# Optimization experiments

Hardware: AMD Instinct MI355X
Metric: run time of the kernel (lower is better)

Reference implementation:

```python
import jax, jax.numpy as jnp
import numpy as np

B, L, D_IN, D_MODEL, D_STATE, D_DISCR, KER = 2, 1024, 512, 1024, 16, 64, 4


def setup_inputs() -> dict:
    ks = jax.random.split(jax.random.key(0), 9)
    s = 0.02
    return {
        "seq": jax.random.normal(ks[0], (B, L, D_IN), jnp.float32),
        "W_in": jax.random.normal(ks[1], (2 * D_MODEL, D_IN), jnp.float32) * s,
        "W_out": jax.random.normal(ks[2], (D_IN, D_MODEL), jnp.float32) * s,
        "W_B": jax.random.normal(ks[3], (D_STATE, D_MODEL), jnp.float32) * s,
        "W_C": jax.random.normal(ks[4], (D_STATE, D_MODEL), jnp.float32) * s,
        "W_D1": jax.random.normal(ks[5], (D_DISCR, D_MODEL), jnp.float32) * s,
        "W_D2": jax.random.normal(ks[6], (D_MODEL, D_DISCR), jnp.float32) * s,
        "conv_w": jax.random.normal(ks[7], (D_MODEL, 1, KER), jnp.float32) * 0.1,
        "conv_b": jax.random.normal(ks[8], (D_MODEL,), jnp.float32) * 0.01,
        "A": jnp.tile(jnp.arange(1, D_STATE + 1, dtype=jnp.float32), (D_MODEL, 1)),
        "D": jnp.ones((D_MODEL,), jnp.float32),
    }


def _causal_depthwise_conv(x, w, b):
    # x: [B, L, D] -> torch Conv1d(groups=D, padding=KER-1) truncated to first L outputs
    x = jnp.swapaxes(x, 1, 2)  # [B, D, L]
    y = jax.lax.conv_general_dilated(
        x, w, window_strides=(1,), padding=[(KER - 1, 0)],
        dimension_numbers=("NCH", "OIH", "NCH"), feature_group_count=D_MODEL)
    y = y + b[None, :, None]
    return jnp.swapaxes(y, 1, 2)  # [B, L, D]


def _ssm(x, W_B, W_C, W_D1, W_D2, A, D):
    # x: [B, L, D]
    exp_negA = jnp.exp(-A)                                  # [D, S]
    Bm = jnp.einsum("bld,sd->bls", x, W_B)                  # [B, L, S]
    Cm = jnp.einsum("bld,sd->bls", x, W_C)                  # [B, L, S]
    delta = jax.nn.softplus(D + jnp.einsum("ble,de->bld", jnp.einsum("bld,ed->ble", x, W_D1), W_D2))  # [B, L, D]
    A_bar = exp_negA[None, None] * delta[..., None]         # [B, L, D, S]
    X = Bm[:, :, None, :] * delta[..., None] * x[..., None]  # [B, L, D, S]

    def comb(c1, c2):
        a1, x1 = c1
        a2, x2 = c2
        return a1 * a2, a2 * x1 + x2

    _, h = jax.lax.associative_scan(comb, (A_bar, X), axis=1)  # h: [B, L, D, S]
    y = jnp.einsum("blds,bls->bld", h, Cm)
    return y + D * x


def reference(seq, W_in, W_out, W_B, W_C, W_D1, W_D2, conv_w, conv_b, A, D):
    ab = jnp.einsum("bli,oi->blo", seq, W_in)   # [B, L, 2*D_MODEL]
    a, b = ab[..., :D_MODEL], ab[..., D_MODEL:]
    a = jax.nn.silu(_causal_depthwise_conv(a, conv_w, conv_b))
    a = _ssm(a, W_B, W_C, W_D1, W_D2, A, D)
    out = a * jax.nn.silu(b)
    return jnp.einsum("bld,od->blo", out, W_out)  # [B, L, D_IN]
```

## Files before the change

kernel.cpp:

```cpp
#include <hip/hip_runtime.h>
#include <hip/hip_bf16.h>

typedef short short8 __attribute__((ext_vector_type(8)));
typedef float float4v __attribute__((ext_vector_type(4)));

#define B_   2
#define L_   1024
#define DIN  512
#define DM   1024
#define DS   16
#define DD   64
#define KER_ 4
#define NROW (B_*L_)

#define SD   8
#define SC   32
#define SLC  32
#define SDP  9

__device__ __forceinline__ float silu_f(float v){ return v / (1.f + expf(-v)); }

__device__ __forceinline__ short2 f2bf2(float a, float b) {
  __hip_bfloat162 h = __float22bfloat162_rn(float2{a, b});
  union { __hip_bfloat162 h; short2 s; } u; u.h = h; return u.s;
}
__device__ __forceinline__ short8 pack8(const float4& x0, const float4& x1) {
  short2 s0 = f2bf2(x0.x, x0.y), s1 = f2bf2(x0.z, x0.w);
  short2 s2 = f2bf2(x1.x, x1.y), s3 = f2bf2(x1.z, x1.w);
  return short8{ s0.x, s0.y, s1.x, s1.y, s2.x, s2.y, s3.x, s3.y };
}

__global__ __launch_bounds__(512)
void gemm1_k(const float* __restrict__ seq, const float* __restrict__ Win,
             float* __restrict__ ab) {
  __shared__ short As[128 * 40];
  __shared__ short Bs[128 * 40];
  const int tid  = threadIdx.x;
  const int lane = tid & 63;
  const int wave = tid >> 6;
  const int r16  = lane & 15;
  const int quad = lane >> 4;
  const int m0 = blockIdx.y * 128;
  const int n0 = blockIdx.x * 128;
  const int wm = wave & 1, wn = wave >> 1;
  float4v acc[4][2];
#pragma unroll
  for (int i = 0; i < 4; i++)
#pragma unroll
    for (int j = 0; j < 2; j++) acc[i][j] = (float4v){0.f, 0.f, 0.f, 0.f};
  float4 pf0[2], pf1[2];
  auto ldu = [&](int j, int k0) {
    int u = tid + j * 512;
    const float4* p;
    if (u < 512) { int row = u >> 2, q = u & 3;
      p = (const float4*)(seq + (size_t)(m0 + row) * DIN + k0 + q * 8);
    } else { int v = u - 512; int row = v >> 2, q = v & 3;
      p = (const float4*)(Win + (size_t)(n0 + row) * DIN + k0 + q * 8);
    }
    pf0[j] = p[0]; pf1[j] = p[1];
  };
  auto stu = [&](int j) {
    int u = tid + j * 512;
    short8 s = pack8(pf0[j], pf1[j]);
    if (u < 512) { int row = u >> 2, q = u & 3; *(short8*)&As[row * 40 + q * 8] = s; }
    else { int v = u - 512; int row = v >> 2, q = v & 3; *(short8*)&Bs[row * 40 + q * 8] = s; }
  };
  ldu(0, 0); ldu(1, 0);
  for (int k0 = 0; k0 < DIN; k0 += 32) {
    stu(0); stu(1);
    __syncthreads();
    if (k0 + 32 < DIN) { ldu(0, k0 + 32); ldu(1, k0 + 32); }
    short8 afr[4], bfr[2];
#pragma unroll
    for (int mi = 0; mi < 4; mi++)
      afr[mi] = *(const short8*)&As[(wm * 64 + mi * 16 + r16) * 40 + quad * 8];
#pragma unroll
    for (int ni = 0; ni < 2; ni++)
      bfr[ni] = *(const short8*)&Bs[(wn * 32 + ni * 16 + r16) * 40 + quad * 8];
#pragma unroll
    for (int mi = 0; mi < 4; mi++)
#pragma unroll
      for (int ni = 0; ni < 2; ni++)
        acc[mi][ni] = __builtin_amdgcn_mfma_f32_16x16x32_bf16(afr[mi], bfr[ni], acc[mi][ni], 0, 0, 0);
    __syncthreads();
  }
#pragma unroll
  for (int mi = 0; mi < 4; mi++)
#pragma unroll
    for (int ni = 0; ni < 2; ni++)
#pragma unroll
      for (int r = 0; r < 4; r++)
        ab[(size_t)(m0 + wm * 64 + mi * 16 + quad * 4 + r) * (2 * DM)
           + n0 + wn * 32 + ni * 16 + r16] = acc[mi][ni][r];
}

__global__ __launch_bounds__(256)
void conv_silu_k(const float* __restrict__ ab, const float* __restrict__ cw,
                 const float* __restrict__ cb, float* __restrict__ x) {
  int idx = blockIdx.x * 256 + threadIdx.x;
  int d  = idx & (DM - 1);
  int n  = idx >> 10;
  int l  = n & (L_ - 1);
  int bb = n >> 10;
  float acc = cb[d];
#pragma unroll
  for (int k = 0; k < KER_; k++) {
    int ll = l - (KER_ - 1) + k;
    if (ll >= 0) acc += ab[(size_t)(bb * L_ + ll) * (2 * DM) + d] * cw[d * KER_ + k];
  }
  x[idx] = silu_f(acc);
}

__global__ __launch_bounds__(256)
void proj_k(const float* __restrict__ x, const float* __restrict__ WB,
            const float* __restrict__ WC, const float* __restrict__ WD1,
            float* __restrict__ pall) {
  __shared__ short As[64 * 40];
  __shared__ short Bs[96 * 40];
  const int tid  = threadIdx.x;
  const int lane = tid & 63;
  const int wave = tid >> 6;
  const int r16  = lane & 15;
  const int quad = lane >> 4;
  const int m0   = blockIdx.y * 64;
  const int kbeg = blockIdx.z * 128;
  float4v acc[6];
#pragma unroll
  for (int i = 0; i < 6; i++) acc[i] = (float4v){0.f, 0.f, 0.f, 0.f};
  float4 pf0[3], pf1[3];
  auto ldu = [&](int j, int k0) {
    int u = tid + j * 256;
    if (u >= 640) return;
    const float4* p;
    if (u < 256) { int row = u >> 2, q = u & 3;
      p = (const float4*)(x + (size_t)(m0 + row) * DM + k0 + q * 8);
    } else { int v = u - 256; int row = v >> 2, q = v & 3;
      const float* bp = (row < 16) ? (WB + (size_t)row * DM)
                      : (row < 32) ? (WC + (size_t)(row - 16) * DM)
                                   : (WD1 + (size_t)(row - 32) * DM);
      p = (const float4*)(bp + k0 + q * 8);
    }
    pf0[j] = p[0]; pf1[j] = p[1];
  };
  auto stu = [&](int j) {
    int u = tid + j * 256;
    if (u >= 640) return;
    short8 s = pack8(pf0[j], pf1[j]);
    if (u < 256) { int row = u >> 2, q = u & 3; *(short8*)&As[row * 40 + q * 8] = s; }
    else { int v = u - 256; int row = v >> 2, q = v & 3; *(short8*)&Bs[row * 40 + q * 8] = s; }
  };
  ldu(0, kbeg); ldu(1, kbeg); ldu(2, kbeg);
  for (int k0 = kbeg; k0 < kbeg + 128; k0 += 32) {
    stu(0); stu(1); stu(2);
    __syncthreads();
    if (k0 + 32 < kbeg + 128) { ldu(0, k0 + 32); ldu(1, k0 + 32); ldu(2, k0 + 32); }
    short8 afr = *(const short8*)&As[(wave * 16 + r16) * 40 + quad * 8];
#pragma unroll
    for (int ni = 0; ni < 6; ni++) {
      short8 bfr = *(const short8*)&Bs[(ni * 16 + r16) * 40 + quad * 8];
      acc[ni] = __builtin_amdgcn_mfma_f32_16x16x32_bf16(afr, bfr, acc[ni], 0, 0, 0);
    }
    __syncthreads();
  }
#pragma unroll
  for (int ni = 0; ni < 6; ni++) {
    int gn = ni * 16 + r16;
#pragma unroll
    for (int r = 0; r < 4; r++) {
      int gm = m0 + wave * 16 + quad * 4 + r;
      atomicAdd(&pall[(size_t)gm * 96 + gn], acc[ni][r]);
    }
  }
}

__global__ __launch_bounds__(256)
void delta_k(const float* __restrict__ t1, const float* __restrict__ WD2,
             const float* __restrict__ Dv, float* __restrict__ dlt) {
  __shared__ short As[64 * 40];
  __shared__ short Bs[64 * 40];
  const int tid  = threadIdx.x;
  const int lane = tid & 63;
  const int wave = tid >> 6;
  const int r16  = lane & 15;
  const int quad = lane >> 4;
  const int m0 = blockIdx.y * 64;
  const int n0 = blockIdx.x * 64;
  const int wm = wave & 1, wn = wave >> 1;
  float4v acc[2][2];
#pragma unroll
  for (int i = 0; i < 2; i++)
#pragma unroll
    for (int j = 0; j < 2; j++) acc[i][j] = (float4v){0.f, 0.f, 0.f, 0.f};
  float4 pf0[2], pf1[2];
  auto ldu = [&](int j, int k0) {
    int u = tid + j * 256;
    const float4* p;
    if (u < 256) { int row = u >> 2, q = u & 3;
      p = (const float4*)(t1 + (size_t)(m0 + row) * 96 + k0 + q * 8);
    } else { int v = u - 256; int row = v >> 2, q = v & 3;
      p = (const float4*)(WD2 + (size_t)(n0 + row) * DD + k0 + q * 8);
    }
    pf0[j] = p[0]; pf1[j] = p[1];
  };
  auto stu = [&](int j) {
    int u = tid + j * 256;
    short8 s = pack8(pf0[j], pf1[j]);
    if (u < 256) { int row = u >> 2, q = u & 3; *(short8*)&As[row * 40 + q * 8] = s; }
    else { int v = u - 256; int row = v >> 2, q = v & 3; *(short8*)&Bs[row * 40 + q * 8] = s; }
  };
  ldu(0, 0); ldu(1, 0);
  for (int k0 = 0; k0 < DD; k0 += 32) {
    stu(0); stu(1);
    __syncthreads();
    if (k0 + 32 < DD) { ldu(0, k0 + 32); ldu(1, k0 + 32); }
    short8 afr[2], bfr[2];
#pragma unroll
    for (int mi = 0; mi < 2; mi++)
      afr[mi] = *(const short8*)&As[(wm * 32 + mi * 16 + r16) * 40 + quad * 8];
#pragma unroll
    for (int ni = 0; ni < 2; ni++)
      bfr[ni] = *(const short8*)&Bs[(wn * 32 + ni * 16 + r16) * 40 + quad * 8];
#pragma unroll
    for (int mi = 0; mi < 2; mi++)
#pragma unroll
      for (int ni = 0; ni < 2; ni++)
        acc[mi][ni] = __builtin_amdgcn_mfma_f32_16x16x32_bf16(afr[mi], bfr[ni], acc[mi][ni], 0, 0, 0);
    __syncthreads();
  }
#pragma unroll
  for (int mi = 0; mi < 2; mi++)
#pragma unroll
    for (int ni = 0; ni < 2; ni++) {
      int gn = n0 + wn * 32 + ni * 16 + r16;
      float dvn = Dv[gn];
#pragma unroll
      for (int r = 0; r < 4; r++) {
        int gm = m0 + wm * 32 + mi * 16 + quad * 4 + r;
        float v = acc[mi][ni][r] + dvn;
        v = fmaxf(v, 0.f) + log1pf(expf(-fabsf(v)));
        dlt[(size_t)gm * DM + gn] = v;
      }
    }
}

__global__ __launch_bounds__(256)
void scan_fused_k(const float* __restrict__ x, const float* __restrict__ dlt,
                  const float* __restrict__ pall, const float* __restrict__ A,
                  const float* __restrict__ Dv, const float* __restrict__ ab,
                  float* __restrict__ sout) {
  __shared__ float Pl[SC][DS][SDP];
  __shared__ float Hl[SC][DS][SDP];
  const int blk = blockIdx.x;
  const int b   = blk >> 7;
  const int d0  = (blk & 127) * SD;
  const int dd  = threadIdx.x & (SD - 1);
  const int c   = threadIdx.x >> 3;
  const int d   = d0 + dd;

  float e[DS];
#pragma unroll
  for (int s = 0; s < DS; s++) e[s] = expf(-A[d * DS + s]);
  const int nbase = b * L_ + c * SLC;

  float h[DS], p[DS];
#pragma unroll
  for (int s = 0; s < DS; s++) { h[s] = 0.f; p[s] = 1.f; }
  for (int i = 0; i < SLC; i++) {
    int n = nbase + i;
    float dl = dlt[(size_t)n * DM + d];
    float xv = x[(size_t)n * DM + d];
    float dx = dl * xv;
    const float4* bm4 = (const float4*)(pall + (size_t)n * 96);
    float4 b0 = bm4[0], b1 = bm4[1], b2 = bm4[2], b3 = bm4[3];
    float bmv[DS] = { b0.x,b0.y,b0.z,b0.w, b1.x,b1.y,b1.z,b1.w,
                      b2.x,b2.y,b2.z,b2.w, b3.x,b3.y,b3.z,b3.w };
#pragma unroll
    for (int s = 0; s < DS; s++) {
      float a_ = e[s] * dl;
      h[s] = a_ * h[s] + bmv[s] * dx;
      p[s] *= a_;
    }
  }
#pragma unroll
  for (int s = 0; s < DS; s++) { Pl[c][s][dd] = p[s]; Hl[c][s][dd] = h[s]; }
  __syncthreads();

  if (threadIdx.x < DS * SD) {
    int s2  = threadIdx.x >> 3;
    int dd2 = threadIdx.x & (SD - 1);
    float H = 0.f;
    for (int c2 = 0; c2 < SC; c2++) {
      float pp = Pl[c2][s2][dd2];
      float hh = Hl[c2][s2][dd2];
      Pl[c2][s2][dd2] = H;
      H = pp * H + hh;
    }
  }
  __syncthreads();

#pragma unroll
  for (int s = 0; s < DS; s++) h[s] = Pl[c][s][dd];
  float Dd = Dv[d];
  for (int i = 0; i < SLC; i++) {
    int n = nbase + i;
    float dl = dlt[(size_t)n * DM + d];
    float xv = x[(size_t)n * DM + d];
    float dx = dl * xv;
    const float4* bm4 = (const float4*)(pall + (size_t)n * 96);
    float4 b0 = bm4[0], b1 = bm4[1], b2 = bm4[2], b3 = bm4[3];
    float4 c0 = bm4[4], c1 = bm4[5], c2v = bm4[6], c3 = bm4[7];
    float bmv[DS] = { b0.x,b0.y,b0.z,b0.w, b1.x,b1.y,b1.z,b1.w,
                      b2.x,b2.y,b2.z,b2.w, b3.x,b3.y,b3.z,b3.w };
    float cmv[DS] = { c0.x,c0.y,c0.z,c0.w, c1.x,c1.y,c1.z,c1.w,
                      c2v.x,c2v.y,c2v.z,c2v.w, c3.x,c3.y,c3.z,c3.w };
    float y = 0.f;
#pragma unroll
    for (int s = 0; s < DS; s++) {
      h[s] = e[s] * dl * h[s] + bmv[s] * dx;
      y += h[s] * cmv[s];
    }
    y += Dd * xv;
    float g = ab[(size_t)n * (2 * DM) + DM + d];
    sout[(size_t)n * DM + d] = y * silu_f(g);
  }
}

__global__ __launch_bounds__(512)
void gemm2_k(const float* __restrict__ sout, const float* __restrict__ Wout,
             float* __restrict__ out) {
  __shared__ short As[64 * 40];
  __shared__ short Bs[64 * 40];
  const int tid  = threadIdx.x;
  const int lane = tid & 63;
  const int wave = tid >> 6;
  const int r16  = lane & 15;
  const int quad = lane >> 4;
  const int m0 = blockIdx.y * 64;
  const int n0 = blockIdx.x * 64;
  const int wm = wave & 1, wn = wave >> 1;
  float4v acc[2];
  acc[0] = (float4v){0.f, 0.f, 0.f, 0.f};
  acc[1] = (float4v){0.f, 0.f, 0.f, 0.f};
  float4 pf0, pf1;
  auto ldu = [&](int k0) {
    const float4* p;
    if (tid < 256) { int row = tid >> 2, q = tid & 3;
      p = (const float4*)(sout + (size_t)(m0 + row) * DM + k0 + q * 8);
    } else { int v = tid - 256; int row = v >> 2, q = v & 3;
      p = (const float4*)(Wout + (size_t)(n0 + row) * DM + k0 + q * 8);
    }
    pf0 = p[0]; pf1 = p[1];
  };
  auto stu = [&]() {
    short8 s = pack8(pf0, pf1);
    if (tid < 256) { int row = tid >> 2, q = tid & 3; *(short8*)&As[row * 40 + q * 8] = s; }
    else { int v = tid - 256; int row = v >> 2, q = v & 3; *(short8*)&Bs[row * 40 + q * 8] = s; }
  };
  ldu(0);
  for (int k0 = 0; k0 < DM; k0 += 32) {
    stu();
    __syncthreads();
    if (k0 + 32 < DM) ldu(k0 + 32);
    short8 afr[2], bfr;
    afr[0] = *(const short8*)&As[(wm * 32 + r16) * 40 + quad * 8];
    afr[1] = *(const short8*)&As[(wm * 32 + 16 + r16) * 40 + quad * 8];
    bfr    = *(const short8*)&Bs[(wn * 16 + r16) * 40 + quad * 8];
    acc[0] = __builtin_amdgcn_mfma_f32_16x16x32_bf16(afr[0], bfr, acc[0], 0, 0, 0);
    acc[1] = __builtin_amdgcn_mfma_f32_16x16x32_bf16(afr[1], bfr, acc[1], 0, 0, 0);
    __syncthreads();
  }
#pragma unroll
  for (int mi = 0; mi < 2; mi++)
#pragma unroll
    for (int r = 0; r < 4; r++)
      out[(size_t)(m0 + wm * 32 + mi * 16 + quad * 4 + r) * DIN + n0 + wn * 16 + r16] = acc[mi][r];
}

extern "C" void kernel_launch(void* const* d_in, const int* in_sizes, int n_in,
                              void* d_out, int out_size, void* d_ws, size_t ws_size,
                              hipStream_t stream) {
  const float* seq  = (const float*)d_in[0];
  const float* Win  = (const float*)d_in[1];
  const float* Wout = (const float*)d_in[2];
  const float* WB   = (const float*)d_in[3];
  const float* WC   = (const float*)d_in[4];
  const float* WD1  = (const float*)d_in[5];
  const float* WD2  = (const float*)d_in[6];
  const float* cw   = (const float*)d_in[7];
  const float* cb   = (const float*)d_in[8];
  const float* A    = (const float*)d_in[9];
  const float* Dv   = (const float*)d_in[10];
  float* out = (float*)d_out;

  float* ws   = (float*)d_ws;
  float* ab   = ws;
  float* x    = ab   + 4194304;
  float* dlt  = x    + 2097152;
  float* pall = dlt  + 2097152;
  float* sout = pall + 196608;
  float* t1   = pall + 32;

  hipMemsetAsync(pall, 0, (size_t)NROW * 96 * 4, stream);
  gemm1_k<<<dim3(16, 16), 512, 0, stream>>>(seq, Win, ab);
  conv_silu_k<<<NROW * DM / 256, 256, 0, stream>>>(ab, cw, cb, x);
  proj_k<<<dim3(1, 32, 8), 256, 0, stream>>>(x, WB, WC, WD1, pall);
  delta_k<<<dim3(16, 32), 256, 0, stream>>>(t1, WD2, Dv, dlt);
  scan_fused_k<<<B_ * (DM / SD), 256, 0, stream>>>(x, dlt, pall, A, Dv, ab, sout);
  gemm2_k<<<dim3(8, 32), 512, 0, stream>>>(sout, Wout, out);
}
```

Baseline: 179.1 us.

## Fuse causal conv+SiLU into projection and scan, store ab in bf16

Drops the standalone conv_silu kernel and its fp32 x buffer. The depthwise causal conv plus SiLU is now recomputed inside proj_k, when staging the A tile, and inside both scan passes, using a rolling three-tap register window. The gemm1 output ab is written as bf16 to halve its traffic, gemm1 moves to 64x64 tiles with 256 threads, and the scan uses 4 channels by 64 chunks per block so there are more blocks. The cost is recomputing the conv in three places and extra bf16 rounding of the gate and conv inputs.

New measurement: 179.9 us. Within noise of the previous version (+0.5%).

```diff
diff --git a/kernel.cpp b/kernel.cpp
--- a/kernel.cpp
+++ b/kernel.cpp
@@ -13,10 +13,10 @@
 #define KER_ 4
 #define NROW (B_*L_)
 
-#define SD   8
-#define SC   32
-#define SLC  32
-#define SDP  9
+#define SD   4
+#define SC   64
+#define SLC  16
+#define SDP  5
 
 __device__ __forceinline__ float silu_f(float v){ return v / (1.f + expf(-v)); }
 
@@ -29,91 +29,81 @@
   short2 s2 = f2bf2(x1.x, x1.y), s3 = f2bf2(x1.z, x1.w);
   return short8{ s0.x, s0.y, s1.x, s1.y, s2.x, s2.y, s3.x, s3.y };
 }
-
-__global__ __launch_bounds__(512)
+__device__ __forceinline__ float bf2f(short s) {
+  union { unsigned u; float f; } v; v.u = ((unsigned)(unsigned short)s) << 16; return v.f;
+}
+
+__global__ __launch_bounds__(256)
 void gemm1_k(const float* __restrict__ seq, const float* __restrict__ Win,
-             float* __restrict__ ab) {
-  __shared__ short As[128 * 40];
-  __shared__ short Bs[128 * 40];
+             __hip_bfloat16* __restrict__ ab) {
+  __shared__ short As[64 * 40];
+  __shared__ short Bs[64 * 40];
   const int tid  = threadIdx.x;
   const int lane = tid & 63;
   const int wave = tid >> 6;
   const int r16  = lane & 15;
   const int quad = lane >> 4;
-  const int m0 = blockIdx.y * 128;
-  const int n0 = blockIdx.x * 128;
+  const int m0 = blockIdx.y * 64;
+  const int n0 = blockIdx.x * 64;
   const int wm = wave & 1, wn = wave >> 1;
-  float4v acc[4][2];
-#pragma unroll
-  for (int i = 0; i < 4; i++)
+  float4v acc[2][2];
+#pragma unroll
+  for (int i = 0; i < 2; i++)
 #pragma unroll
     for (int j = 0; j < 2; j++) acc[i][j] = (float4v){0.f, 0.f, 0.f, 0.f};
   float4 pf0[2], pf1[2];
   auto ldu = [&](int j, int k0) {
-    int u = tid + j * 512;
+    int u = tid + j * 256;
     const float4* p;
-    if (u < 512) { int row = u >> 2, q = u & 3;
+    if (u < 256) { int row = u >> 2, q = u & 3;
       p = (const float4*)(seq + (size_t)(m0 + row) * DIN + k0 + q * 8);
-    } else { int v = u - 512; int row = v >> 2, q = v & 3;
+    } else { int v = u - 256; int row = v >> 2, q = v & 3;
       p = (const float4*)(Win + (size_t)(n0 + row) * DIN + k0 + q * 8);
     }
     pf0[j] = p[0]; pf1[j] = p[1];
   };
   auto stu = [&](int j) {
-    int u = tid + j * 512;
+    int u = tid + j * 256;
     short8 s = pack8(pf0[j], pf1[j]);
-    if (u < 512) { int row = u >> 2, q = u & 3; *(short8*)&As[row * 40 + q * 8] = s; }
-    else { int v = u - 512; int row = v >> 2, q = v & 3; *(short8*)&Bs[row * 40 + q * 8] = s; }
+    if (u < 256) { int row = u >> 2, q = u & 3; *(short8*)&As[row * 40 + q * 8] = s; }
+    else { int v = u - 256; int row = v >> 2, q = v & 3; *(short8*)&Bs[row * 40 + q * 8] = s; }
   };
   ldu(0, 0); ldu(1, 0);
   for (int k0 = 0; k0 < DIN; k0 += 32) {
     stu(0); stu(1);
     __syncthreads();
     if (k0 + 32 < DIN) { ldu(0, k0 + 32); ldu(1, k0 + 32); }
-    short8 afr[4], bfr[2];
-#pragma unroll
-    for (int mi = 0; mi < 4; mi++)
-      afr[mi] = *(const short8*)&As[(wm * 64 + mi * 16 + r16) * 40 + quad * 8];
+    short8 afr[2], bfr[2];
+#pragma unroll
+    for (int mi = 0; mi < 2; mi++)
+      afr[mi] = *(const short8*)&As[(wm * 32 + mi * 16 + r16) * 40 + quad * 8];
 #pragma unroll
     for (int ni = 0; ni < 2; ni++)
       bfr[ni] = *(const short8*)&Bs[(wn * 32 + ni * 16 + r16) * 40 + quad * 8];
 #pragma unroll
-    for (int mi = 0; mi < 4; mi++)
+    for (int mi = 0; mi < 2; mi++)
 #pragma unroll
       for (int ni = 0; ni < 2; ni++)
         acc[mi][ni] = __builtin_amdgcn_mfma_f32_16x16x32_bf16(afr[mi], bfr[ni], acc[mi][ni], 0, 0, 0);
     __syncthreads();
   }
 #pragma unroll
-  for (int mi = 0; mi < 4; mi++)
-#pragma unroll
-    for (int ni = 0; ni < 2; ni++)
-#pragma unroll
-      for (int r = 0; r < 4; r++)
-        ab[(size_t)(m0 + wm * 64 + mi * 16 + quad * 4 + r) * (2 * DM)
-           + n0 + wn * 32 + ni * 16 + r16] = acc[mi][ni][r];
+  for (int mi = 0; mi < 2; mi++)
+#pragma unroll
+    for (int ni = 0; ni < 2; ni++) {
+      int gn = n0 + wn * 32 + ni * 16 + r16;
+#pragma unroll
+      for (int r = 0; r < 4; r++) {
+        int gm = m0 + wm * 32 + mi * 16 + quad * 4 + r;
+        ab[(size_t)gm * (2 * DM) + gn] = __float2bfloat16(acc[mi][ni][r]);
+      }
+    }
 }
 
 __global__ __launch_bounds__(256)
-void conv_silu_k(const float* __restrict__ ab, const float* __restrict__ cw,
-                 const float* __restrict__ cb, float* __restrict__ x) {
-  int idx = blockIdx.x * 256 + threadIdx.x;
-  int d  = idx & (DM - 1);
-  int n  = idx >> 10;
-  int l  = n & (L_ - 1);
-  int bb = n >> 10;
-  float acc = cb[d];
-#pragma unroll
-  for (int k = 0; k < KER_; k++) {
-    int ll = l - (KER_ - 1) + k;
-    if (ll >= 0) acc += ab[(size_t)(bb * L_ + ll) * (2 * DM) + d] * cw[d * KER_ + k];
-  }
-  x[idx] = silu_f(acc);
-}
-
-__global__ __launch_bounds__(256)
-void proj_k(const float* __restrict__ x, const float* __restrict__ WB,
+void proj_k(const __hip_bfloat16* __restrict__ ab, const float* __restrict__ WB,
             const float* __restrict__ WC, const float* __restrict__ WD1,
+            const float* __restrict__ cw, const float* __restrict__ cb,
             float* __restrict__ pall) {
   __shared__ short As[64 * 40];
   __shared__ short Bs[96 * 40];
@@ -127,33 +117,61 @@
   float4v acc[6];
 #pragma unroll
   for (int i = 0; i < 6; i++) acc[i] = (float4v){0.f, 0.f, 0.f, 0.f};
-  float4 pf0[3], pf1[3];
-  auto ldu = [&](int j, int k0) {
+
+  short8 ta[KER_];
+  float4 pf0[2], pf1[2];
+
+  const int arow = tid >> 2, aq = tid & 3;
+  const int an = m0 + arow, al = an & (L_ - 1), abq = an >> 10;
+
+  auto ldu_a = [&](int k0) {
+#pragma unroll
+    for (int t = 0; t < KER_; t++) {
+      int ll = al - (KER_ - 1) + t;
+      if (ll >= 0)
+        ta[t] = *(const short8*)(ab + (size_t)(abq * L_ + ll) * (2 * DM) + k0 + aq * 8);
+      else
+        ta[t] = short8{0,0,0,0,0,0,0,0};
+    }
+  };
+  auto stu_a = [&](int k0) {
+    float r8[8];
+#pragma unroll
+    for (int e = 0; e < 8; e++) {
+      int d = k0 + aq * 8 + e;
+      float4 w = *(const float4*)(cw + d * 4);
+      float a = cb[d];
+      a += bf2f(ta[0][e]) * w.x;
+      a += bf2f(ta[1][e]) * w.y;
+      a += bf2f(ta[2][e]) * w.z;
+      a += bf2f(ta[3][e]) * w.w;
+      r8[e] = silu_f(a);
+    }
+    *(short8*)&As[arow * 40 + aq * 8] =
+        pack8(float4{r8[0], r8[1], r8[2], r8[3]}, float4{r8[4], r8[5], r8[6], r8[7]});
+  };
+  auto ldu_b = [&](int j, int k0) {
     int u = tid + j * 256;
     if (u >= 640) return;
-    const float4* p;
-    if (u < 256) { int row = u >> 2, q = u & 3;
-      p = (const float4*)(x + (size_t)(m0 + row) * DM + k0 + q * 8);
-    } else { int v = u - 256; int row = v >> 2, q = v & 3;
-      const float* bp = (row < 16) ? (WB + (size_t)row * DM)
-                      : (row < 32) ? (WC + (size_t)(row - 16) * DM)
-                                   : (WD1 + (size_t)(row - 32) * DM);
-      p = (const float4*)(bp + k0 + q * 8);
-    }
-    pf0[j] = p[0]; pf1[j] = p[1];
-  };
-  auto stu = [&](int j) {
+    int v = u - 256, row = v >> 2, q = v & 3;
+    const float* bp = (row < 16) ? (WB + (size_t)row * DM)
+                    : (row < 32) ? (WC + (size_t)(row - 16) * DM)
+                                 : (WD1 + (size_t)(row - 32) * DM);
+    const float4* p = (const float4*)(bp + k0 + q * 8);
+    pf0[j - 1] = p[0]; pf1[j - 1] = p[1];
+  };
+  auto stu_b = [&](int j) {
     int u = tid + j * 256;
     if (u >= 640) return;
-    short8 s = pack8(pf0[j], pf1[j]);
-    if (u < 256) { int row = u >> 2, q = u & 3; *(short8*)&As[row * 40 + q * 8] = s; }
-    else { int v = u - 256; int row = v >> 2, q = v & 3; *(short8*)&Bs[row * 40 + q * 8] = s; }
-  };
-  ldu(0, kbeg); ldu(1, kbeg); ldu(2, kbeg);
+    int v = u - 256, row = v >> 2, q = v & 3;
+    *(short8*)&Bs[row * 40 + q * 8] = pack8(pf0[j - 1], pf1[j - 1]);
+  };
+
+  ldu_a(kbeg); ldu_b(1, kbeg); ldu_b(2, kbeg);
   for (int k0 = kbeg; k0 < kbeg + 128; k0 += 32) {
-    stu(0); stu(1); stu(2);
-    __syncthreads();
-    if (k0 + 32 < kbeg + 128) { ldu(0, k0 + 32); ldu(1, k0 + 32); ldu(2, k0 + 32); }
+    stu_a(k0); stu_b(1); stu_b(2);
+    __syncthreads();
+    if (k0 + 32 < kbeg + 128) { ldu_a(k0 + 32); ldu_b(1, k0 + 32); ldu_b(2, k0 + 32); }
     short8 afr = *(const short8*)&As[(wave * 16 + r16) * 40 + quad * 8];
 #pragma unroll
     for (int ni = 0; ni < 6; ni++) {
@@ -244,31 +262,41 @@
 }
 
 __global__ __launch_bounds__(256)
-void scan_fused_k(const float* __restrict__ x, const float* __restrict__ dlt,
+void scan_fused_k(const __hip_bfloat16* __restrict__ ab, const float* __restrict__ dlt,
                   const float* __restrict__ pall, const float* __restrict__ A,
-                  const float* __restrict__ Dv, const float* __restrict__ ab,
-                  float* __restrict__ sout) {
+                  const float* __restrict__ Dv, const float* __restrict__ cw,
+                  const float* __restrict__ cb, float* __restrict__ sout) {
   __shared__ float Pl[SC][DS][SDP];
   __shared__ float Hl[SC][DS][SDP];
   const int blk = blockIdx.x;
-  const int b   = blk >> 7;
-  const int d0  = (blk & 127) * SD;
+  const int b   = blk >> 8;
+  const int d0  = (blk & 255) * SD;
   const int dd  = threadIdx.x & (SD - 1);
-  const int c   = threadIdx.x >> 3;
+  const int c   = threadIdx.x >> 2;
   const int d   = d0 + dd;
 
   float e[DS];
 #pragma unroll
   for (int s = 0; s < DS; s++) e[s] = expf(-A[d * DS + s]);
-  const int nbase = b * L_ + c * SLC;
-
+  const int   lbase = c * SLC;
+  const int   nbase = b * L_ + lbase;
+  const float4 w    = *(const float4*)(cw + d * 4);
+  const float  cbv  = cb[d];
+
+  auto abA = [&](int l) -> float {
+    return (l >= 0) ? __bfloat162float(ab[(size_t)(b * L_ + l) * (2 * DM) + d]) : 0.f;
+  };
+
+  float r0 = abA(lbase - 3), r1 = abA(lbase - 2), r2 = abA(lbase - 1);
   float h[DS], p[DS];
 #pragma unroll
   for (int s = 0; s < DS; s++) { h[s] = 0.f; p[s] = 1.f; }
   for (int i = 0; i < SLC; i++) {
     int n = nbase + i;
+    float a3 = __bfloat162float(ab[(size_t)n * (2 * DM) + d]);
+    float xv = silu_f(cbv + r0 * w.x + r1 * w.y + r2 * w.z + a3 * w.w);
+    r0 = r1; r1 = r2; r2 = a3;
     float dl = dlt[(size_t)n * DM + d];
-    float xv = x[(size_t)n * DM + d];
     float dx = dl * xv;
     const float4* bm4 = (const float4*)(pall + (size_t)n * 96);
     float4 b0 = bm4[0], b1 = bm4[1], b2 = bm4[2], b3 = bm4[3];
@@ -286,7 +314,7 @@
   __syncthreads();
 
   if (threadIdx.x < DS * SD) {
-    int s2  = threadIdx.x >> 3;
+    int s2  = threadIdx.x >> 2;
     int dd2 = threadIdx.x & (SD - 1);
     float H = 0.f;
     for (int c2 = 0; c2 < SC; c2++) {
@@ -301,10 +329,13 @@
 #pragma unroll
   for (int s = 0; s < DS; s++) h[s] = Pl[c][s][dd];
   float Dd = Dv[d];
+  r0 = abA(lbase - 3); r1 = abA(lbase - 2); r2 = abA(lbase - 1);
   for (int i = 0; i < SLC; i++) {
     int n = nbase + i;
+    float a3 = __bfloat162float(ab[(size_t)n * (2 * DM) + d]);
+    float xv = silu_f(cbv + r0 * w.x + r1 * w.y + r2 * w.z + a3 * w.w);
+    r0 = r1; r1 = r2; r2 = a3;
     float dl = dlt[(size_t)n * DM + d];
-    float xv = x[(size_t)n * DM + d];
     float dx = dl * xv;
     const float4* bm4 = (const float4*)(pall + (size_t)n * 96);
     float4 b0 = bm4[0], b1 = bm4[1], b2 = bm4[2], b3 = bm4[3];
@@ -320,7 +351,7 @@
       y += h[s] * cmv[s];
     }
     y += Dd * xv;
-    float g = ab[(size_t)n * (2 * DM) + DM + d];
+    float g = __bfloat162float(ab[(size_t)n * (2 * DM) + DM + d]);
     sout[(size_t)n * DM + d] = y * silu_f(g);
   }
 }
@@ -392,19 +423,17 @@
   const float* Dv   = (const float*)d_in[10];
   float* out = (float*)d_out;
 
-  float* ws   = (float*)d_ws;
-  float* ab   = ws;
-  float* x    = ab   + 4194304;
-  float* dlt  = x    + 2097152;
+  float* ws = (float*)d_ws;
+  __hip_bfloat16* ab = (__hip_bfloat16*)ws;
+  float* dlt  = ws   + 2097152;
   float* pall = dlt  + 2097152;
   float* sout = pall + 196608;
   float* t1   = pall + 32;
 
   hipMemsetAsync(pall, 0, (size_t)NROW * 96 * 4, stream);
-  gemm1_k<<<dim3(16, 16), 512, 0, stream>>>(seq, Win, ab);
-  conv_silu_k<<<NROW * DM / 256, 256, 0, stream>>>(ab, cw, cb, x);
-  proj_k<<<dim3(1, 32, 8), 256, 0, stream>>>(x, WB, WC, WD1, pall);
+  gemm1_k<<<dim3(32, 32), 256, 0, stream>>>(seq, Win, ab);
+  proj_k<<<dim3(1, 32, 8), 256, 0, stream>>>(ab, WB, WC, WD1, cw, cb, pall);
   delta_k<<<dim3(16, 32), 256, 0, stream>>>(t1, WD2, Dv, dlt);
-  scan_fused_k<<<B_ * (DM / SD), 256, 0, stream>>>(x, dlt, pall, A, Dv, ab, sout);
+  scan_fused_k<<<B_ * (DM / SD), 256, 0, stream>>>(ab, dlt, pall, A, Dv, cw, cb, sout);
   gemm2_k<<<dim3(8, 32), 512, 0, stream>>>(sout, Wout, out);
 }
```
